# Performance work log

Measured on AMD Instinct MI355X. Metric: run time of the kernel, lower is better.

## Reference

```python
import jax, jax.numpy as jnp
import numpy as np

N_NODES = 100000
N_EDGES = 1600000
F_IN = 128
F_OUT = 64


def setup_inputs() -> dict:
    key = jax.random.key(0)
    kx, kw, kv, ks, kd = jax.random.split(key, 5)
    x = jax.random.normal(kx, (N_NODES, F_IN), dtype=jnp.float32)
    # xavier_uniform init for weight [in, out]
    limit = float(np.sqrt(6.0 / (F_IN + F_OUT)))
    weight = jax.random.uniform(kw, (F_IN, F_OUT), dtype=jnp.float32,
                                minval=-limit, maxval=limit)
    edge_val = jax.random.uniform(kv, (N_EDGES,), dtype=jnp.float32)
    edge_src = jax.random.randint(ks, (N_EDGES,), 0, N_NODES, dtype=jnp.int64)
    edge_dst = jax.random.randint(kd, (N_EDGES,), 0, N_NODES, dtype=jnp.int64)
    return {"x": x, "weight": weight, "edge_val": edge_val,
            "edge_src": edge_src, "edge_dst": edge_dst}


def reference(x, weight, edge_val, edge_src, edge_dst):
    # dropout p = 0.0 -> identity
    support = x @ weight                                  # [N, F_OUT] dense GEMM
    # spmm: out[dst] += val * support[src]  (adj row = dst, col = src)
    messages = support[edge_src] * edge_val[:, None]       # [E, F_OUT] gather
    out = jax.ops.segment_sum(messages, edge_dst,
                              num_segments=x.shape[0])     # [N, F_OUT] scatter-add
    return jax.nn.relu(out)
```

## Files before the change

### kernel.cpp

```cpp
#include <hip/hip_runtime.h>

#define F_IN 128
#define F_OUT 64
#define GROWS 128
#define XBSTRIDE 136

#define NPB 128
#define NPB_SHIFT 7
#define BCAP 800
#define ECAP 2560
#define TILE 8192
#define BSTH 1024
#define TMAX 256

__device__ inline unsigned f2bf(float f) {
    const unsigned u = __float_as_uint(f);
    return (u + 0x7FFFu + ((u >> 16) & 1u)) >> 16;
}
__device__ inline float bf_lo(unsigned u) { return __uint_as_float(u << 16); }
__device__ inline float bf_hi(unsigned u) { return __uint_as_float(u & 0xFFFF0000u); }

struct GemmSh {
    float4 w[F_IN * F_OUT / 4];
    unsigned short xt[GROWS * XBSTRIDE];
};
struct ScatSh {
    int2 ebuf2[TILE];
    int  h[BCAP];
    int  lcur[BCAP];
    int  wsum[16];
    int  woff[16];
};
union FusedSh { GemmSh g; ScatSh s; };

__global__ __launch_bounds__(BSTH) void fused_kernel(const float* __restrict__ x,
                                                     const float* __restrict__ w,
                                                     unsigned short* __restrict__ support,
                                                     int n_nodes,
                                                     const float* __restrict__ edge_val,
                                                     const int* __restrict__ edge_src,
                                                     const int* __restrict__ edge_dst,
                                                     int* __restrict__ toff,
                                                     int2* __restrict__ sorted,
                                                     int n_edges, int nb, int T) {
    __shared__ FusedSh u;
    const int tid = threadIdx.x;

    if ((int)blockIdx.x >= T) {
        const int row0 = (blockIdx.x - T) * GROWS;

        {
            const float4* w4 = (const float4*)w;
            #pragma unroll
            for (int i = tid; i < F_IN * F_OUT / 4; i += BSTH) u.g.w[i] = w4[i];
        }
        {
            const float4* x4 = (const float4*)x;
            #pragma unroll
            for (int i = tid; i < GROWS * (F_IN / 8); i += BSTH) {
                const int r  = i >> 4;
                const int k8 = i & 15;
                const int row = row0 + r;
                float4 a = make_float4(0.f, 0.f, 0.f, 0.f);
                float4 b = make_float4(0.f, 0.f, 0.f, 0.f);
                if (row < n_nodes) {
                    a = x4[(size_t)row * (F_IN / 4) + 2 * k8 + 0];
                    b = x4[(size_t)row * (F_IN / 4) + 2 * k8 + 1];
                }
                uint4 o;
                o.x = f2bf(a.x) | (f2bf(a.y) << 16);
                o.y = f2bf(a.z) | (f2bf(a.w) << 16);
                o.z = f2bf(b.x) | (f2bf(b.y) << 16);
                o.w = f2bf(b.z) | (f2bf(b.w) << 16);
                *(uint4*)&u.g.xt[r * XBSTRIDE + k8 * 8] = o;
            }
        }
        __syncthreads();

        const int tf = tid & 15;
        const int tr = tid >> 4;

        float acc[2][4] = {};
        #pragma unroll 2
        for (int k8 = 0; k8 < F_IN / 8; ++k8) {
            const uint4 xa = *(const uint4*)&u.g.xt[tr * XBSTRIDE + k8 * 8];
            const uint4 xb = *(const uint4*)&u.g.xt[(tr + 64) * XBSTRIDE + k8 * 8];
            float xA[8], xB[8];
            xA[0] = bf_lo(xa.x); xA[1] = bf_hi(xa.x); xA[2] = bf_lo(xa.y); xA[3] = bf_hi(xa.y);
            xA[4] = bf_lo(xa.z); xA[5] = bf_hi(xa.z); xA[6] = bf_lo(xa.w); xA[7] = bf_hi(xa.w);
            xB[0] = bf_lo(xb.x); xB[1] = bf_hi(xb.x); xB[2] = bf_lo(xb.y); xB[3] = bf_hi(xb.y);
            xB[4] = bf_lo(xb.z); xB[5] = bf_hi(xb.z); xB[6] = bf_lo(xb.w); xB[7] = bf_hi(xb.w);
            #pragma unroll
            for (int j = 0; j < 8; ++j) {
                const float4 wv = u.g.w[(8 * k8 + j) * 16 + tf];
                acc[0][0] += xA[j] * wv.x; acc[0][1] += xA[j] * wv.y;
                acc[0][2] += xA[j] * wv.z; acc[0][3] += xA[j] * wv.w;
                acc[1][0] += xB[j] * wv.x; acc[1][1] += xB[j] * wv.y;
                acc[1][2] += xB[j] * wv.z; acc[1][3] += xB[j] * wv.w;
            }
        }
        #pragma unroll
        for (int i = 0; i < 2; ++i) {
            const int row = row0 + tr + 64 * i;
            if (row < n_nodes) {
                ushort4 o;
                o.x = (unsigned short)f2bf(acc[i][0]);
                o.y = (unsigned short)f2bf(acc[i][1]);
                o.z = (unsigned short)f2bf(acc[i][2]);
                o.w = (unsigned short)f2bf(acc[i][3]);
                *(ushort4*)&support[(size_t)row * F_OUT + 4 * tf] = o;
            }
        }
        return;
    }

    const int te  = blockIdx.x * TILE;
    const int cnt = min(TILE, n_edges - te);

    for (int i = tid; i < BCAP; i += BSTH) u.s.h[i] = 0;
    __syncthreads();

    const int cnt4 = cnt >> 2;
    const int4*   s4 = (const int4*)(edge_src + te);
    const int4*   d4 = (const int4*)(edge_dst + te);
    const float4* v4 = (const float4*)(edge_val + te);
    int4 rs[2], rd[2]; float4 rv[2];
    #pragma unroll
    for (int it = 0; it < 2; ++it) {
        const int t = tid + it * BSTH;
        if (t < cnt4) {
            rs[it] = s4[t]; rd[it] = d4[t]; rv[it] = v4[t];
            atomicAdd(&u.s.h[rd[it].x >> NPB_SHIFT], 1);
            atomicAdd(&u.s.h[rd[it].y >> NPB_SHIFT], 1);
            atomicAdd(&u.s.h[rd[it].z >> NPB_SHIFT], 1);
            atomicAdd(&u.s.h[rd[it].w >> NPB_SHIFT], 1);
        }
    }
    if (tid == 0) {
        for (int e = cnt4 << 2; e < cnt; ++e)
            atomicAdd(&u.s.h[edge_dst[te + e] >> NPB_SHIFT], 1);
    }
    __syncthreads();

    const int v = (tid < nb) ? u.s.h[tid] : 0;
    int s = v;
    #pragma unroll
    for (int off = 1; off < 64; off <<= 1) {
        const int t = __shfl_up(s, off, 64);
        if ((tid & 63) >= off) s += t;
    }
    const int wave = tid >> 6;
    if ((tid & 63) == 63) u.s.wsum[wave] = s;
    __syncthreads();
    if (tid < 16) {
        const int ws = u.s.wsum[tid];
        int sc = ws;
        #pragma unroll
        for (int off = 1; off < 16; off <<= 1) {
            const int t = __shfl_up(sc, off, 64);
            if (tid >= off) sc += t;
        }
        u.s.woff[tid] = sc - ws;
    }
    __syncthreads();

    int* trow = toff + (size_t)blockIdx.x * (nb + 1);
    if (tid < nb) {
        const int start = s + u.s.woff[wave] - v;
        u.s.lcur[tid] = start;
        trow[tid] = start;
    }
    if (tid == 0) trow[nb] = cnt;
    __syncthreads();

    #pragma unroll
    for (int it = 0; it < 2; ++it) {
        const int t = tid + it * BSTH;
        if (t < cnt4) {
            int b, r;
            b = rd[it].x >> NPB_SHIFT; r = atomicAdd(&u.s.lcur[b], 1);
            u.s.ebuf2[r] = make_int2(rs[it].x | ((rd[it].x & (NPB - 1)) << 20), __float_as_int(rv[it].x));
            b = rd[it].y >> NPB_SHIFT; r = atomicAdd(&u.s.lcur[b], 1);
            u.s.ebuf2[r] = make_int2(rs[it].y | ((rd[it].y & (NPB - 1)) << 20), __float_as_int(rv[it].y));
            b = rd[it].z >> NPB_SHIFT; r = atomicAdd(&u.s.lcur[b], 1);
            u.s.ebuf2[r] = make_int2(rs[it].z | ((rd[it].z & (NPB - 1)) << 20), __float_as_int(rv[it].z));
            b = rd[it].w >> NPB_SHIFT; r = atomicAdd(&u.s.lcur[b], 1);
            u.s.ebuf2[r] = make_int2(rs[it].w | ((rd[it].w & (NPB - 1)) << 20), __float_as_int(rv[it].w));
        }
    }
    if (tid == 0) {
        for (int e = cnt4 << 2; e < cnt; ++e) {
            const int dd = edge_dst[te + e];
            const int b = dd >> NPB_SHIFT;
            const int r = atomicAdd(&u.s.lcur[b], 1);
            u.s.ebuf2[r] = make_int2(edge_src[te + e] | ((dd & (NPB - 1)) << 20),
                                     __float_as_int(edge_val[te + e]));
        }
    }
    __syncthreads();

    for (int k = tid; k < cnt; k += BSTH)
        sorted[(size_t)te + k] = u.s.ebuf2[k];
}

__global__ __launch_bounds__(512) void baccum_kernel(const unsigned short* __restrict__ support,
                                                     const int2* __restrict__ sorted,
                                                     const int* __restrict__ toff,
                                                     float* __restrict__ out,
                                                     int n_nodes, int T, int nb) {
    __shared__ int2 ebuf[ECAP];
    __shared__ int2 ebuf2[ECAP];
    __shared__ int tstart[TMAX];
    __shared__ int toffb[TMAX];
    __shared__ int wsum3[4];
    __shared__ int total_s;
    __shared__ int hist[NPB];
    __shared__ int node_off[NPB + 1];
    __shared__ int cursor[NPB];
    __shared__ int wsum2[2];

    const int tid = threadIdx.x;
    const int b = blockIdx.x;

    int mycnt = 0, myoff = 0;
    if (tid < TMAX) {
        if (tid < T) {
            const int s0 = toff[(size_t)tid * (nb + 1) + b];
            const int e0 = toff[(size_t)tid * (nb + 1) + b + 1];
            toffb[tid] = s0;
            mycnt = e0 - s0;
        }
        int s = mycnt;
        #pragma unroll
        for (int off = 1; off < 64; off <<= 1) {
            const int t = __shfl_up(s, off, 64);
            if ((tid & 63) >= off) s += t;
        }
        if ((tid & 63) == 63) wsum3[tid >> 6] = s;
        myoff = s - mycnt;
    }
    __syncthreads();
    if (tid < TMAX && tid < T) {
        int add = 0;
        const int wv = tid >> 6;
        for (int q2 = 0; q2 < wv; ++q2) add += wsum3[q2];
        tstart[tid] = myoff + add;
    }
    if (tid == 0) total_s = wsum3[0] + wsum3[1] + wsum3[2] + wsum3[3];
    __syncthreads();
    const int total = total_s;

    const int g8 = tid >> 3;
    const int q  = tid & 7;
    const uint4* sup = (const uint4*)support;

    float4 accA[2], accB[2];
    #pragma unroll
    for (int j = 0; j < 2; ++j) {
        accA[j] = make_float4(0.f, 0.f, 0.f, 0.f);
        accB[j] = make_float4(0.f, 0.f, 0.f, 0.f);
    }

    for (int cb = 0; cb < total; cb += ECAP) {
        const int cnt = min(ECAP, total - cb);

        __syncthreads();
        if (tid < NPB) hist[tid] = 0;
        __syncthreads();

        for (int i = tid; i < cnt; i += 512) {
            const int g = cb + i;
            int lo = 0, hi = T - 1;
            while (lo < hi) {
                const int mid = (lo + hi + 1) >> 1;
                if (tstart[mid] <= g) lo = mid; else hi = mid - 1;
            }
            const int2 ev = sorted[(size_t)lo * TILE + toffb[lo] + (g - tstart[lo])];
            ebuf[i] = ev;
            atomicAdd(&hist[((unsigned)ev.x) >> 20], 1);
        }
        __syncthreads();

        {
            int v = 0;
            if (tid < NPB) v = hist[tid];
            int s = v;
            if (tid < NPB) {
                #pragma unroll
                for (int off = 1; off < 64; off <<= 1) {
                    const int t = __shfl_up(s, off, 64);
                    if ((tid & 63) >= off) s += t;
                }
                if ((tid & 63) == 63) wsum2[tid >> 6] = s;
            }
            __syncthreads();
            if (tid < NPB) {
                const int incl = s + ((tid >= 64) ? wsum2[0] : 0);
                node_off[tid + 1] = incl;
                cursor[tid] = incl - v;
                if (tid == 0) node_off[0] = 0;
            }
        }
        __syncthreads();

        for (int i = tid; i < cnt; i += 512) {
            const int2 ev = ebuf[i];
            const int r = atomicAdd(&cursor[((unsigned)ev.x) >> 20], 1);
            ebuf2[r] = ev;
        }
        __syncthreads();

        #pragma unroll
        for (int j = 0; j < 2; ++j) {
            const int nl = g8 + 64 * j;
            int k = node_off[nl];
            const int ke = node_off[nl + 1];
            float4 aA = accA[j], aB = accB[j];
            while (k + 8 <= ke) {
                int2 e[8];
                uint4 s[8];
                #pragma unroll
                for (int u2 = 0; u2 < 8; ++u2) e[u2] = ebuf2[k + u2];
                #pragma unroll
                for (int u2 = 0; u2 < 8; ++u2)
                    s[u2] = sup[(size_t)(e[u2].x & 0xFFFFF) * 8 + q];
                #pragma unroll
                for (int u2 = 0; u2 < 8; ++u2) {
                    const float v = __int_as_float(e[u2].y);
                    aA.x += v * bf_lo(s[u2].x); aA.y += v * bf_hi(s[u2].x);
                    aA.z += v * bf_lo(s[u2].y); aA.w += v * bf_hi(s[u2].y);
                    aB.x += v * bf_lo(s[u2].z); aB.y += v * bf_hi(s[u2].z);
                    aB.z += v * bf_lo(s[u2].w); aB.w += v * bf_hi(s[u2].w);
                }
                k += 8;
            }
            for (; k < ke; ++k) {
                const int2 e0 = ebuf2[k];
                const uint4 s0 = sup[(size_t)(e0.x & 0xFFFFF) * 8 + q];
                const float v0 = __int_as_float(e0.y);
                aA.x += v0 * bf_lo(s0.x); aA.y += v0 * bf_hi(s0.x);
                aA.z += v0 * bf_lo(s0.y); aA.w += v0 * bf_hi(s0.y);
                aB.x += v0 * bf_lo(s0.z); aB.y += v0 * bf_hi(s0.z);
                aB.z += v0 * bf_lo(s0.w); aB.w += v0 * bf_hi(s0.w);
            }
            accA[j] = aA; accB[j] = aB;
        }
    }

    const int base = b << NPB_SHIFT;
    #pragma unroll
    for (int j = 0; j < 2; ++j) {
        const int node = base + g8 + 64 * j;
        if (node < n_nodes) {
            float4 vA = accA[j], vB = accB[j];
            vA.x = fmaxf(vA.x, 0.f); vA.y = fmaxf(vA.y, 0.f);
            vA.z = fmaxf(vA.z, 0.f); vA.w = fmaxf(vA.w, 0.f);
            vB.x = fmaxf(vB.x, 0.f); vB.y = fmaxf(vB.y, 0.f);
            vB.z = fmaxf(vB.z, 0.f); vB.w = fmaxf(vB.w, 0.f);
            ((float4*)out)[(size_t)node * 16 + 2 * q + 0] = vA;
            ((float4*)out)[(size_t)node * 16 + 2 * q + 1] = vB;
        }
    }
}

__global__ __launch_bounds__(256) void scatter_kernel(const unsigned short* __restrict__ support,
                                                      const float* __restrict__ edge_val,
                                                      const int* __restrict__ edge_src,
                                                      const int* __restrict__ edge_dst,
                                                      float* __restrict__ out,
                                                      int n_edges) {
    const long gid = (long)blockIdx.x * blockDim.x + threadIdx.x;
    const int e = (int)(gid >> 4);
    if (e >= n_edges) return;
    const int q = (int)(gid & 15);
    const int src   = edge_src[e];
    const int dst   = edge_dst[e];
    const float val = edge_val[e];
    const uint2 s = ((const uint2*)support)[(size_t)src * 16 + q];
    float* o = &out[(size_t)dst * F_OUT + q * 4];
    atomicAdd(o + 0, val * bf_lo(s.x));
    atomicAdd(o + 1, val * bf_hi(s.x));
    atomicAdd(o + 2, val * bf_lo(s.y));
    atomicAdd(o + 3, val * bf_hi(s.y));
}

__global__ __launch_bounds__(256) void relu_kernel(float* __restrict__ out, int n4) {
    const int i = blockIdx.x * blockDim.x + threadIdx.x;
    if (i < n4) {
        float4 v = ((float4*)out)[i];
        v.x = fmaxf(v.x, 0.f); v.y = fmaxf(v.y, 0.f);
        v.z = fmaxf(v.z, 0.f); v.w = fmaxf(v.w, 0.f);
        ((float4*)out)[i] = v;
    }
}

extern "C" void kernel_launch(void* const* d_in, const int* in_sizes, int n_in,
                              void* d_out, int out_size, void* d_ws, size_t ws_size,
                              hipStream_t stream) {
    const float* x        = (const float*)d_in[0];
    const float* w        = (const float*)d_in[1];
    const float* edge_val = (const float*)d_in[2];
    const int*   edge_src = (const int*)d_in[3];
    const int*   edge_dst = (const int*)d_in[4];
    float* out = (float*)d_out;

    const int n_nodes = in_sizes[0] / F_IN;
    const int n_edges = in_sizes[2];
    const int nb = (n_nodes + NPB - 1) >> NPB_SHIFT;
    const int T  = (n_edges + TILE - 1) / TILE;
    const int G  = (n_nodes + GROWS - 1) / GROWS;

    char* p = (char*)d_ws;
    unsigned short* support = (unsigned short*)p;
    p += (size_t)n_nodes * F_OUT * sizeof(unsigned short);
    p = (char*)(((size_t)p + 15) & ~(size_t)15);
    int2* sorted = (int2*)p;  p += (size_t)T * TILE * sizeof(int2);
    int*  toff   = (int*)p;   p += (size_t)T * (nb + 1) * sizeof(int);
    const size_t ws_needed = (size_t)(p - (char*)d_ws);

    const bool ok = (ws_size >= ws_needed) && (nb <= BCAP) && (n_nodes < (1 << 20))
                    && (T <= TMAX);
    if (ok) {
        fused_kernel<<<T + G, BSTH, 0, stream>>>(x, w, support, n_nodes,
                                                 edge_val, edge_src, edge_dst,
                                                 toff, sorted, n_edges, nb, T);
        baccum_kernel<<<nb, 512, 0, stream>>>(support, sorted, toff, out,
                                              n_nodes, T, nb);
    } else {
        fused_kernel<<<G, BSTH, 0, stream>>>(x, w, support, n_nodes,
                                             edge_val, edge_src, edge_dst,
                                             nullptr, nullptr, n_edges, nb, 0);
        hipMemsetAsync(d_out, 0, (size_t)out_size * sizeof(float), stream);
        const long st = (long)n_edges * 16;
        scatter_kernel<<<(int)((st + 255) / 256), 256, 0, stream>>>(
            support, edge_val, edge_src, edge_dst, out, n_edges);
        const int n4o = out_size / 4;
        relu_kernel<<<(n4o + 255) / 256, 256, 0, stream>>>(out, n4o);
    }
}
```

Baseline: 167.7 us.

## Use bf16 MFMA with split hi/lo weights for the fused GEMM blocks

Replaces the scalar FMA GEMM over bf16-converted x with MFMA 16x16x32 bf16 instructions. The weights are stored transposed in shared memory as high and low bf16 parts so the product keeps near-fp32 weight precision. Each of the 16 wavefronts computes a 16x32 output tile. The goal is to cut the ALU cost of the GEMM blocks. In exchange it adds two-term MFMA work, scalar 2-byte global stores, and a smaller ECAP constant that may affect scatter-block capacity.

```diff
diff --git a/kernel.cpp b/kernel.cpp
--- a/kernel.cpp
+++ b/kernel.cpp
@@ -8,7 +8,7 @@
 #define NPB 128
 #define NPB_SHIFT 7
 #define BCAP 800
-#define ECAP 2560
+#define ECAP 2240
 #define TILE 8192
 #define BSTH 1024
 #define TMAX 256
@@ -20,9 +20,13 @@
 __device__ inline float bf_lo(unsigned u) { return __uint_as_float(u << 16); }
 __device__ inline float bf_hi(unsigned u) { return __uint_as_float(u & 0xFFFF0000u); }
 
+using bf16x8 = __attribute__((ext_vector_type(8))) short;
+using f32x4  = __attribute__((ext_vector_type(4))) float;
+
 struct GemmSh {
-    float4 w[F_IN * F_OUT / 4];
     unsigned short xt[GROWS * XBSTRIDE];
+    unsigned short wth[F_OUT * XBSTRIDE];
+    unsigned short wtl[F_OUT * XBSTRIDE];
 };
 struct ScatSh {
     int2 ebuf2[TILE];
@@ -50,9 +54,26 @@
         const int row0 = (blockIdx.x - T) * GROWS;
 
         {
-            const float4* w4 = (const float4*)w;
             #pragma unroll
-            for (int i = tid; i < F_IN * F_OUT / 4; i += BSTH) u.g.w[i] = w4[i];
+            for (int i = tid; i < F_OUT * (F_IN / 8); i += BSTH) {
+                const int col = i & 63;
+                const int kb  = (i >> 6) << 3;
+                unsigned short sh[8], sl[8];
+                #pragma unroll
+                for (int j = 0; j < 8; ++j) {
+                    const float f = w[(size_t)(kb + j) * F_OUT + col];
+                    const unsigned h = f2bf(f);
+                    sh[j] = (unsigned short)h;
+                    sl[j] = (unsigned short)f2bf(f - __uint_as_float(h << 16));
+                }
+                uint4 oh, ol;
+                oh.x = sh[0] | ((unsigned)sh[1] << 16); oh.y = sh[2] | ((unsigned)sh[3] << 16);
+                oh.z = sh[4] | ((unsigned)sh[5] << 16); oh.w = sh[6] | ((unsigned)sh[7] << 16);
+                ol.x = sl[0] | ((unsigned)sl[1] << 16); ol.y = sl[2] | ((unsigned)sl[3] << 16);
+                ol.z = sl[4] | ((unsigned)sl[5] << 16); ol.w = sl[6] | ((unsigned)sl[7] << 16);
+                *(uint4*)&u.g.wth[col * XBSTRIDE + kb] = oh;
+                *(uint4*)&u.g.wtl[col * XBSTRIDE + kb] = ol;
+            }
         }
         {
             const float4* x4 = (const float4*)x;
@@ -77,38 +98,41 @@
         }
         __syncthreads();
 
-        const int tf = tid & 15;
-        const int tr = tid >> 4;
-
-        float acc[2][4] = {};
-        #pragma unroll 2
-        for (int k8 = 0; k8 < F_IN / 8; ++k8) {
-            const uint4 xa = *(const uint4*)&u.g.xt[tr * XBSTRIDE + k8 * 8];
-            const uint4 xb = *(const uint4*)&u.g.xt[(tr + 64) * XBSTRIDE + k8 * 8];
-            float xA[8], xB[8];
-            xA[0] = bf_lo(xa.x); xA[1] = bf_hi(xa.x); xA[2] = bf_lo(xa.y); xA[3] = bf_hi(xa.y);
-            xA[4] = bf_lo(xa.z); xA[5] = bf_hi(xa.z); xA[6] = bf_lo(xa.w); xA[7] = bf_hi(xa.w);
-            xB[0] = bf_lo(xb.x); xB[1] = bf_hi(xb.x); xB[2] = bf_lo(xb.y); xB[3] = bf_hi(xb.y);
-            xB[4] = bf_lo(xb.z); xB[5] = bf_hi(xb.z); xB[6] = bf_lo(xb.w); xB[7] = bf_hi(xb.w);
-            #pragma unroll
-            for (int j = 0; j < 8; ++j) {
-                const float4 wv = u.g.w[(8 * k8 + j) * 16 + tf];
-                acc[0][0] += xA[j] * wv.x; acc[0][1] += xA[j] * wv.y;
-                acc[0][2] += xA[j] * wv.z; acc[0][3] += xA[j] * wv.w;
-                acc[1][0] += xB[j] * wv.x; acc[1][1] += xB[j] * wv.y;
-                acc[1][2] += xB[j] * wv.z; acc[1][3] += xB[j] * wv.w;
-            }
-        }
+        const int ln = tid & 63;
+        const int wv = tid >> 6;
+        const int rt = wv >> 1;
+        const int cp = (wv & 1) << 1;
+        const int lr = ln >> 4;
+        const int lc = ln & 15;
+
+        const unsigned short* ar  = &u.g.xt [(rt * 16 + lc) * XBSTRIDE + lr * 8];
+        const unsigned short* bh0 = &u.g.wth[(cp * 16 + lc) * XBSTRIDE + lr * 8];
+        const unsigned short* bh1 = &u.g.wth[((cp + 1) * 16 + lc) * XBSTRIDE + lr * 8];
+        const unsigned short* bl0 = &u.g.wtl[(cp * 16 + lc) * XBSTRIDE + lr * 8];
+        const unsigned short* bl1 = &u.g.wtl[((cp + 1) * 16 + lc) * XBSTRIDE + lr * 8];
+
+        f32x4 acc0 = {0.f, 0.f, 0.f, 0.f};
+        f32x4 acc1 = {0.f, 0.f, 0.f, 0.f};
         #pragma unroll
-        for (int i = 0; i < 2; ++i) {
-            const int row = row0 + tr + 64 * i;
+        for (int kc = 0; kc < 4; ++kc) {
+            const bf16x8 a  = *(const bf16x8*)(ar  + kc * 32);
+            const bf16x8 h0 = *(const bf16x8*)(bh0 + kc * 32);
+            const bf16x8 h1 = *(const bf16x8*)(bh1 + kc * 32);
+            const bf16x8 l0 = *(const bf16x8*)(bl0 + kc * 32);
+            const bf16x8 l1 = *(const bf16x8*)(bl1 + kc * 32);
+            acc0 = __builtin_amdgcn_mfma_f32_16x16x32_bf16(a, h0, acc0, 0, 0, 0);
+            acc1 = __builtin_amdgcn_mfma_f32_16x16x32_bf16(a, h1, acc1, 0, 0, 0);
+            acc0 = __builtin_amdgcn_mfma_f32_16x16x32_bf16(a, l0, acc0, 0, 0, 0);
+            acc1 = __builtin_amdgcn_mfma_f32_16x16x32_bf16(a, l1, acc1, 0, 0, 0);
+        }
+
+        #pragma unroll
+        for (int i = 0; i < 4; ++i) {
+            const int row = row0 + rt * 16 + lr * 4 + i;
             if (row < n_nodes) {
-                ushort4 o;
-                o.x = (unsigned short)f2bf(acc[i][0]);
-                o.y = (unsigned short)f2bf(acc[i][1]);
-                o.z = (unsigned short)f2bf(acc[i][2]);
-                o.w = (unsigned short)f2bf(acc[i][3]);
-                *(ushort4*)&support[(size_t)row * F_OUT + 4 * tf] = o;
+                unsigned short* sp = &support[(size_t)row * F_OUT + lc];
+                sp[cp * 16]       = (unsigned short)f2bf(acc0[i]);
+                sp[(cp + 1) * 16] = (unsigned short)f2bf(acc1[i]);
             }
         }
         return;
```

Measured after the change: 154.1 us. 8.1% less time.
